# Optimization experiments

Measured on AMD Instinct MI355X. Metric: run time of the kernel, lower is better.

Reference implementation:

```python
import jax, jax.numpy as jnp
import numpy as np

LODS = [16, 32, 64, 128, 256]
SCENE_SCALE = 4.0
DESC = 4
N = 2_000_000
# 8 corner offsets of a voxel, bit-decoded: (x, y, z) in {0,1}^3
_CORNERS = jnp.asarray([[(i >> 2) & 1, (i >> 1) & 1, i & 1] for i in range(8)], dtype=jnp.int32)  # (8,3)


def setup_inputs() -> dict:
    key = jax.random.key(0)
    ks = jax.random.split(key, 2 + len(LODS))
    inp = {
        "pts": jax.random.normal(ks[0], (N, 3), dtype=jnp.float32),
        "d": jax.random.normal(ks[1], (N, 3), dtype=jnp.float32),
    }
    # codebook init mirrors torch: zeros + 0.01 * randn, shape (LOD^3, desc)
    for i, res in enumerate(LODS):
        inp[f"codebook_{i}"] = jax.random.normal(ks[2 + i], (res ** 3, DESC), dtype=jnp.float32) * 0.01
    return inp


def _trilerp(res, codebook, pts01):
    """NGLOD-style dense-grid trilinear interpolation.
    pts01: (N,3) in [0,1]; codebook: (res^3, DESC). Returns (N, DESC)."""
    pos = pts01 * (res - 1)                                   # (N,3) in [0, res-1]
    c0 = jnp.clip(jnp.floor(pos).astype(jnp.int32), 0, res - 2)
    frac = pos - c0.astype(pos.dtype)                         # (N,3) in [0,1]
    idx = c0[:, None, :] + _CORNERS[None, :, :]               # (N,8,3)
    flat = (idx[..., 0] * res + idx[..., 1]) * res + idx[..., 2]  # (N,8) row-major x*res^2+y*res+z
    # trilinear weights: prod over axes of (frac if corner bit set else 1-frac)
    w = jnp.prod(jnp.where(_CORNERS[None] == 1, frac[:, None, :], 1.0 - frac[:, None, :]), axis=-1)  # (N,8)
    return jnp.einsum('nkd,nk->nd', codebook[flat], w)        # gather + weighted sum


def reference(pts, d, codebook_0, codebook_1, codebook_2, codebook_3, codebook_4):
    cbs = (codebook_0, codebook_1, codebook_2, codebook_3, codebook_4)
    p = pts / SCENE_SCALE
    mask = jnp.all(jnp.abs(p) < 0.5, axis=-1)                 # inside unit cube
    p01 = jnp.clip(p + 0.5, 0.0, 1.0)                         # clamp keeps OOB points index-safe; masked out below
    feats = _trilerp(LODS[0], cbs[0], p01)
    for res, cb in zip(LODS[1:], cbs[1:]):
        feats = feats + _trilerp(res, cb, p01)                # sum features across LODs
    color = jnp.where(mask[:, None], feats[:, 0:3], 0.0)      # masked scatter into zero buffer
    log_sigma = jnp.where(mask, feats[:, 3], -100000.0)       # exp(-1e5) underflows to 0, as in torch
    return color, jnp.exp(log_sigma)[:, None]
```

## Files before the change

kernel.cpp:

```cpp
#include <hip/hip_runtime.h>
#include <math.h>

static constexpr float kSceneScale = 4.0f;
static constexpr int   kG     = 16;
static constexpr int   kNBins = kG * kG * kG + 1;
static constexpr int   kNB    = 256;
static constexpr int   kDirectThresh = 48;
static constexpr int   kS4    = 17;
static constexpr int   kChunk = 512;

__device__ __forceinline__ void fma4(float4& acc, float w, const float4& c) {
    acc.x = fmaf(w, c.x, acc.x);
    acc.y = fmaf(w, c.y, acc.y);
    acc.z = fmaf(w, c.z, acc.z);
    acc.w = fmaf(w, c.w, acc.w);
}

__device__ __forceinline__ unsigned bf16r(float f) {
    unsigned u = __float_as_uint(f);
    return (u + 0x7FFFu + ((u >> 16) & 1u)) >> 16;
}
__device__ __forceinline__ unsigned pk2(float lo, float hi) {
    return bf16r(lo) | (bf16r(hi) << 16);
}
__device__ __forceinline__ float4 bfdec(uint2 w) {
    float4 r;
    r.x = __uint_as_float(w.x << 16);
    r.y = __uint_as_float(w.x & 0xFFFF0000u);
    r.z = __uint_as_float(w.y << 16);
    r.w = __uint_as_float(w.y & 0xFFFF0000u);
    return r;
}

template <int RES>
__device__ __forceinline__ void trilerp_acc(const float4* __restrict__ cb,
                                            float x, float y, float z,
                                            float4& acc) {
    const float s = (float)(RES - 1);
    float fx = x * s, fy = y * s, fz = z * s;
    int x0 = min((int)fx, RES - 2);
    int y0 = min((int)fy, RES - 2);
    int z0 = min((int)fz, RES - 2);
    float tx = fx - (float)x0;
    float ty = fy - (float)y0;
    float tz = fz - (float)z0;
    int base = (x0 * RES + y0) * RES + z0;
    float4 c000 = cb[base];
    float4 c001 = cb[base + 1];
    float4 c010 = cb[base + RES];
    float4 c011 = cb[base + RES + 1];
    float4 c100 = cb[base + RES * RES];
    float4 c101 = cb[base + RES * RES + 1];
    float4 c110 = cb[base + RES * RES + RES];
    float4 c111 = cb[base + RES * RES + RES + 1];
    float wx0 = 1.0f - tx, wx1 = tx;
    float wy0 = 1.0f - ty, wy1 = ty;
    float wz0 = 1.0f - tz, wz1 = tz;
    fma4(acc, wx0 * wy0 * wz0, c000);
    fma4(acc, wx0 * wy0 * wz1, c001);
    fma4(acc, wx0 * wy1 * wz0, c010);
    fma4(acc, wx0 * wy1 * wz1, c011);
    fma4(acc, wx1 * wy0 * wz0, c100);
    fma4(acc, wx1 * wy0 * wz1, c101);
    fma4(acc, wx1 * wy1 * wz0, c110);
    fma4(acc, wx1 * wy1 * wz1, c111);
}

__device__ __forceinline__ void load_p01(const float* __restrict__ pts, int i,
                                         float& x, float& y, float& z, bool& inside) {
    float px = pts[3 * i + 0] * (1.0f / kSceneScale);
    float py = pts[3 * i + 1] * (1.0f / kSceneScale);
    float pz = pts[3 * i + 2] * (1.0f / kSceneScale);
    inside = (fabsf(px) < 0.5f) && (fabsf(py) < 0.5f) && (fabsf(pz) < 0.5f);
    x = fminf(fmaxf(px + 0.5f, 0.0f), 1.0f);
    y = fminf(fmaxf(py + 0.5f, 0.0f), 1.0f);
    z = fminf(fmaxf(pz + 0.5f, 0.0f), 1.0f);
}

__device__ __forceinline__ unsigned point_key(const float* __restrict__ pts, int i) {
    float x, y, z; bool inside;
    load_p01(pts, i, x, y, z, inside);
    if (!inside) return (unsigned)(kNBins - 1);
    int x0 = min((int)(x * 255.0f), 254) >> 4;
    int y0 = min((int)(y * 255.0f), 254) >> 4;
    int z0 = min((int)(z * 255.0f), 254) >> 4;
    return (unsigned)((x0 * kG + y0) * kG + z0);
}

__global__ __launch_bounds__(256) void keys_hist_kernel(
        const float* __restrict__ pts, unsigned* __restrict__ keys,
        unsigned* __restrict__ blockHist, int n, int chunk) {
    __shared__ unsigned hist[kNBins];
    int tid = threadIdx.x;
    for (int j = tid; j < kNBins; j += 256) hist[j] = 0;
    __syncthreads();
    int beg = blockIdx.x * chunk;
    int end = min(n, beg + chunk);
    for (int i = beg + tid; i < end; i += 256) {
        unsigned key = point_key(pts, i);
        keys[i] = key;
        atomicAdd(&hist[key], 1u);
    }
    __syncthreads();
    for (int j = tid; j < kNBins; j += 256) blockHist[(size_t)j * kNB + blockIdx.x] = hist[j];
}

__global__ __launch_bounds__(256) void scan_chunks_kernel(
        unsigned* __restrict__ data, unsigned* __restrict__ partials, int total) {
    __shared__ unsigned sums[256];
    int tid = threadIdx.x;
    int base = blockIdx.x * 1024 + tid * 4;
    uint4 v = make_uint4(0u, 0u, 0u, 0u);
    if (base + 3 < total) {
        v = *(const uint4*)(data + base);
    } else {
        unsigned* p = (unsigned*)&v;
        for (int k = 0; k < 4; ++k) if (base + k < total) p[k] = data[base + k];
    }
    unsigned s1 = v.x + v.y, s2 = s1 + v.z, s3 = s2 + v.w;
    sums[tid] = s3;
    __syncthreads();
    for (int off = 1; off < 256; off <<= 1) {
        unsigned t = (tid >= off) ? sums[tid - off] : 0u;
        __syncthreads();
        sums[tid] += t;
        __syncthreads();
    }
    unsigned excl = sums[tid] - s3;
    uint4 o;
    o.x = excl; o.y = excl + v.x; o.z = excl + s1; o.w = excl + s2;
    if (base + 3 < total) {
        *(uint4*)(data + base) = o;
    } else {
        unsigned* p = (unsigned*)&o;
        for (int k = 0; k < 4; ++k) if (base + k < total) data[base + k] = p[k];
    }
    if (tid == 255) partials[blockIdx.x] = sums[255];
}

__global__ __launch_bounds__(256) void scan_partials_kernel(unsigned* __restrict__ partials, int m) {
    __shared__ unsigned buf[256];
    __shared__ unsigned carry_s;
    int tid = threadIdx.x;
    if (tid == 0) carry_s = 0u;
    __syncthreads();
    for (int base = 0; base < m; base += 256) {
        unsigned v = (base + tid < m) ? partials[base + tid] : 0u;
        buf[tid] = v;
        __syncthreads();
        for (int off = 1; off < 256; off <<= 1) {
            unsigned t = (tid >= off) ? buf[tid - off] : 0u;
            __syncthreads();
            buf[tid] += t;
            __syncthreads();
        }
        unsigned incl = buf[tid];
        unsigned c = carry_s;
        if (base + tid < m) partials[base + tid] = c + incl - v;
        __syncthreads();
        if (tid == 255) carry_s = c + incl;
        __syncthreads();
    }
}

__global__ __launch_bounds__(256) void scan_add_kernel(
        unsigned* __restrict__ data, const unsigned* __restrict__ partials, int total) {
    int tid = threadIdx.x;
    int base = blockIdx.x * 1024 + tid * 4;
    unsigned p = partials[blockIdx.x];
    if (base + 3 < total) {
        uint4 v = *(const uint4*)(data + base);
        v.x += p; v.y += p; v.z += p; v.w += p;
        *(uint4*)(data + base) = v;
    } else {
        for (int k = 0; k < 4; ++k) if (base + k < total) data[base + k] += p;
    }
}

__global__ __launch_bounds__(256) void scatter_kernel(
        const float* __restrict__ pts,
        const unsigned* __restrict__ keys, const unsigned* __restrict__ blockHist,
        float4* __restrict__ spts, float* __restrict__ out, int n, int chunk) {
    __shared__ unsigned offs[kNBins];
    int tid = threadIdx.x;
    for (int j = tid; j < kNBins; j += 256) offs[j] = blockHist[(size_t)j * kNB + blockIdx.x];
    __syncthreads();
    int beg = blockIdx.x * chunk;
    int end = min(n, beg + chunk);
    for (int i = beg + tid; i < end; i += 256) {
        unsigned k = keys[i];
        float x, y, z; bool inside;
        load_p01(pts, i, x, y, z, inside);
        unsigned pos = atomicAdd(&offs[k], 1u);
        if (inside) {
            spts[pos] = make_float4(x, y, z, __uint_as_float((unsigned)i));
        } else {
            out[3 * i + 0] = 0.0f;
            out[3 * i + 1] = 0.0f;
            out[3 * i + 2] = 0.0f;
            out[(size_t)3 * n + i] = 0.0f;
        }
    }
}

__global__ __launch_bounds__(512) void build_work_kernel(
        const unsigned* __restrict__ blockHist,
        uint2* __restrict__ items, unsigned* __restrict__ numItems) {
    __shared__ unsigned counter;
    if (threadIdx.x == 0) counter = 0u;
    __syncthreads();
    for (int bin = threadIdx.x; bin < kG * kG * kG; bin += 512) {
        unsigned s = blockHist[(size_t)bin * kNB];
        unsigned e = blockHist[(size_t)(bin + 1) * kNB];
        unsigned cnt = e - s;
        if (cnt == 0u) continue;
        unsigned k = (cnt + kChunk - 1) / kChunk;
        unsigned base = atomicAdd(&counter, k);
        for (unsigned j = 0; j < k; ++j)
            items[base + j] = make_uint2((unsigned)bin, s + j * kChunk);
    }
    __syncthreads();
    if (threadIdx.x == 0) numItems[0] = counter;
}

__global__ __launch_bounds__(512, 8) void compute_tiled_kernel(
        const float4* __restrict__ spts,
        const unsigned* __restrict__ blockHist,
        const uint2* __restrict__ items,
        const unsigned* __restrict__ numItems,
        const float4* __restrict__ cb0,
        const float4* __restrict__ cb1,
        const float4* __restrict__ cb2,
        const float4* __restrict__ cb3,
        const float4* __restrict__ cb4,
        float* __restrict__ out,
        int n) {
    if (blockIdx.x >= numItems[0]) return;
    uint2 it = items[blockIdx.x];
    int bin = (int)it.x;
    unsigned start = it.y;
    unsigned binEnd = blockHist[(size_t)(bin + 1) * kNB];
    unsigned end = min(binEnd, start + (unsigned)kChunk);

    int tid = threadIdx.x;

    if ((int)(end - start) < kDirectThresh) {
        for (unsigned t = start + tid; t < end; t += 512) {
            float4 s = spts[t];
            int i = (int)__float_as_uint(s.w);
            float4 acc = make_float4(0.0f, 0.0f, 0.0f, 0.0f);
            trilerp_acc<16>(cb0, s.x, s.y, s.z, acc);
            trilerp_acc<32>(cb1, s.x, s.y, s.z, acc);
            trilerp_acc<64>(cb2, s.x, s.y, s.z, acc);
            trilerp_acc<128>(cb3, s.x, s.y, s.z, acc);
            trilerp_acc<256>(cb4, s.x, s.y, s.z, acc);
            out[3 * i + 0] = acc.x;
            out[3 * i + 1] = acc.y;
            out[3 * i + 2] = acc.z;
            out[(size_t)3 * n + i] = expf(acc.w);
        }
        return;
    }

    __shared__ uint2 s4[kS4 * kS4 * kS4];

    int bx = bin >> 8, by = (bin >> 4) & 15, bz = bin & 15;
    int ox = bx << 4, oy = by << 4, oz = bz << 4;

    for (int c = tid; c < kS4 * kS4 * kS4; c += 512) {
        int cz = c % kS4;
        int cy = (c / kS4) % kS4;
        int cx = c / (kS4 * kS4);
        int gx = min(ox + cx, 255);
        int gy = min(oy + cy, 255);
        int gz = min(oz + cz, 255);
        float4 v = cb4[((size_t)gx * 256 + gy) * 256 + gz];
        s4[c] = make_uint2(pk2(v.x, v.y), pk2(v.z, v.w));
    }
    __syncthreads();

    unsigned t = start + tid;
    if (t < end) {
        float4 s = spts[t];
        int i = (int)__float_as_uint(s.w);
        float4 acc = make_float4(0.0f, 0.0f, 0.0f, 0.0f);
        trilerp_acc<16>(cb0, s.x, s.y, s.z, acc);
        trilerp_acc<32>(cb1, s.x, s.y, s.z, acc);
        trilerp_acc<64>(cb2, s.x, s.y, s.z, acc);
        trilerp_acc<128>(cb3, s.x, s.y, s.z, acc);

        {
            float fx = s.x * 255.0f, fy = s.y * 255.0f, fz = s.z * 255.0f;
            int x0 = min((int)fx, 254);
            int y0 = min((int)fy, 254);
            int z0 = min((int)fz, 254);
            float tx = fx - (float)x0;
            float ty = fy - (float)y0;
            float tz = fz - (float)z0;
            int base = ((x0 - ox) * kS4 + (y0 - oy)) * kS4 + (z0 - oz);
            uint2 w000 = s4[base];
            uint2 w001 = s4[base + 1];
            uint2 w010 = s4[base + kS4];
            uint2 w011 = s4[base + kS4 + 1];
            uint2 w100 = s4[base + kS4 * kS4];
            uint2 w101 = s4[base + kS4 * kS4 + 1];
            uint2 w110 = s4[base + kS4 * kS4 + kS4];
            uint2 w111 = s4[base + kS4 * kS4 + kS4 + 1];
            float wx0 = 1.0f - tx, wx1 = tx;
            float wy0 = 1.0f - ty, wy1 = ty;
            float wz0 = 1.0f - tz, wz1 = tz;
            fma4(acc, wx0 * wy0 * wz0, bfdec(w000));
            fma4(acc, wx0 * wy0 * wz1, bfdec(w001));
            fma4(acc, wx0 * wy1 * wz0, bfdec(w010));
            fma4(acc, wx0 * wy1 * wz1, bfdec(w011));
            fma4(acc, wx1 * wy0 * wz0, bfdec(w100));
            fma4(acc, wx1 * wy0 * wz1, bfdec(w101));
            fma4(acc, wx1 * wy1 * wz0, bfdec(w110));
            fma4(acc, wx1 * wy1 * wz1, bfdec(w111));
        }

        out[3 * i + 0] = acc.x;
        out[3 * i + 1] = acc.y;
        out[3 * i + 2] = acc.z;
        out[(size_t)3 * n + i] = expf(acc.w);
    }
}

__global__ __launch_bounds__(256) void direct_kernel(
        const float* __restrict__ pts,
        const float4* __restrict__ cb0,
        const float4* __restrict__ cb1,
        const float4* __restrict__ cb2,
        const float4* __restrict__ cb3,
        const float4* __restrict__ cb4,
        float* __restrict__ out,
        int n) {
    int i = blockIdx.x * blockDim.x + threadIdx.x;
    if (i >= n) return;
    float x, y, z; bool inside;
    load_p01(pts, i, x, y, z, inside);
    float c0 = 0.0f, c1 = 0.0f, c2 = 0.0f, sg = 0.0f;
    if (inside) {
        float4 acc = make_float4(0.0f, 0.0f, 0.0f, 0.0f);
        trilerp_acc<16>(cb0, x, y, z, acc);
        trilerp_acc<32>(cb1, x, y, z, acc);
        trilerp_acc<64>(cb2, x, y, z, acc);
        trilerp_acc<128>(cb3, x, y, z, acc);
        trilerp_acc<256>(cb4, x, y, z, acc);
        c0 = acc.x; c1 = acc.y; c2 = acc.z; sg = expf(acc.w);
    }
    out[3 * i + 0] = c0;
    out[3 * i + 1] = c1;
    out[3 * i + 2] = c2;
    out[(size_t)3 * n + i] = sg;
}

extern "C" void kernel_launch(void* const* d_in, const int* in_sizes, int n_in,
                              void* d_out, int out_size, void* d_ws, size_t ws_size,
                              hipStream_t stream) {
    const float* pts = (const float*)d_in[0];
    const float4* cb0 = (const float4*)d_in[2];
    const float4* cb1 = (const float4*)d_in[3];
    const float4* cb2 = (const float4*)d_in[4];
    const float4* cb3 = (const float4*)d_in[5];
    const float4* cb4 = (const float4*)d_in[6];
    float* out = (float*)d_out;

    int n = in_sizes[0] / 3;

    const int histTotal = kNBins * kNB;
    const int nChunks   = (histTotal + 1023) / 1024;
    const int maxItems  = kG * kG * kG + (n + kChunk - 1) / kChunk;

    size_t off_keys  = 0;
    size_t off_spts  = (off_keys + (size_t)n * 4 + 15) & ~(size_t)15;
    size_t off_hist  = off_spts + (size_t)n * 16;
    size_t off_part  = off_hist + (size_t)histTotal * 4;
    size_t off_items = (off_part + (size_t)nChunks * 4 + 7) & ~(size_t)7;
    size_t off_nitem = off_items + (size_t)maxItems * 8;
    size_t need      = off_nitem + 4;

    dim3 block(256);
    int nwg = (n + 255) / 256;

    if (ws_size < need) {
        direct_kernel<<<dim3(nwg), block, 0, stream>>>(pts, cb0, cb1, cb2, cb3, cb4, out, n);
        return;
    }

    unsigned* keys      = (unsigned*)((char*)d_ws + off_keys);
    float4*   spts      = (float4*)((char*)d_ws + off_spts);
    unsigned* blockHist = (unsigned*)((char*)d_ws + off_hist);
    unsigned* partials  = (unsigned*)((char*)d_ws + off_part);
    uint2*    items     = (uint2*)((char*)d_ws + off_items);
    unsigned* numItems  = (unsigned*)((char*)d_ws + off_nitem);

    int chunk = (n + kNB - 1) / kNB;

    keys_hist_kernel<<<dim3(kNB), block, 0, stream>>>(pts, keys, blockHist, n, chunk);
    scan_chunks_kernel<<<dim3(nChunks), block, 0, stream>>>(blockHist, partials, histTotal);
    scan_partials_kernel<<<dim3(1), block, 0, stream>>>(partials, nChunks);
    scan_add_kernel<<<dim3(nChunks), block, 0, stream>>>(blockHist, partials, histTotal);
    scatter_kernel<<<dim3(kNB), block, 0, stream>>>(pts, keys, blockHist, spts, out, n, chunk);
    build_work_kernel<<<dim3(1), dim3(512), 0, stream>>>(blockHist, items, numItems);
    compute_tiled_kernel<<<dim3(maxItems), dim3(512), 0, stream>>>(
        spts, blockHist, items, numItems, cb0, cb1, cb2, cb3, cb4, out, n);
}
```

Baseline: 303.7 us.

## Stage all LOD codebook tiles in LDS and halve bin depth along z

The spatial bins are split twice as finely along z, with 8-voxel depth instead of 16. Each tiled block now stages bf16-packed codebook windows for all five LODs into shared memory, not only the finest one. The trilinear lookups for every level then read from LDS instead of issuing scattered global gathers for LODs 0-3. The trade-offs are twice as many histogram bins to scan, more staging work per block relative to its point count, and bf16 rounding on every level rather than just the finest.

```diff
diff --git a/kernel.cpp b/kernel.cpp
--- a/kernel.cpp
+++ b/kernel.cpp
@@ -2,11 +2,11 @@
 #include <math.h>
 
 static constexpr float kSceneScale = 4.0f;
-static constexpr int   kG     = 16;
-static constexpr int   kNBins = kG * kG * kG + 1;
+static constexpr int   kGX    = 16;
+static constexpr int   kGZ    = 32;
+static constexpr int   kNBins = kGX * kGX * kGZ + 1;
 static constexpr int   kNB    = 256;
 static constexpr int   kDirectThresh = 48;
-static constexpr int   kS4    = 17;
 static constexpr int   kChunk = 512;
 
 __device__ __forceinline__ void fma4(float4& acc, float w, const float4& c) {
@@ -83,8 +83,8 @@
     if (!inside) return (unsigned)(kNBins - 1);
     int x0 = min((int)(x * 255.0f), 254) >> 4;
     int y0 = min((int)(y * 255.0f), 254) >> 4;
-    int z0 = min((int)(z * 255.0f), 254) >> 4;
-    return (unsigned)((x0 * kG + y0) * kG + z0);
+    int z0 = min((int)(z * 255.0f), 254) >> 3;
+    return (unsigned)((x0 * kGX + y0) * kGZ + z0);
 }
 
 __global__ __launch_bounds__(256) void keys_hist_kernel(
@@ -209,7 +209,7 @@
     __shared__ unsigned counter;
     if (threadIdx.x == 0) counter = 0u;
     __syncthreads();
-    for (int bin = threadIdx.x; bin < kG * kG * kG; bin += 512) {
+    for (int bin = threadIdx.x; bin < kGX * kGX * kGZ; bin += 512) {
         unsigned s = blockHist[(size_t)bin * kNB];
         unsigned e = blockHist[(size_t)(bin + 1) * kNB];
         unsigned cnt = e - s;
@@ -222,6 +222,62 @@
     __syncthreads();
     if (threadIdx.x == 0) numItems[0] = counter;
 }
+
+template <int RES, int SX, int SZ>
+__device__ __forceinline__ void stage_lds(const float4* __restrict__ cb, uint2* sbuf,
+                                          int lox, int loy, int loz, int tid) {
+    constexpr int TOT = SX * SX * SZ;
+    for (int c = tid; c < TOT; c += 512) {
+        int cz = c % SZ;
+        int cy = (c / SZ) % SX;
+        int cx = c / (SZ * SX);
+        int gx = min(lox + cx, RES - 1);
+        int gy = min(loy + cy, RES - 1);
+        int gz = min(loz + cz, RES - 1);
+        float4 v = cb[((size_t)gx * RES + gy) * RES + gz];
+        sbuf[c] = make_uint2(pk2(v.x, v.y), pk2(v.z, v.w));
+    }
+}
+
+template <int RES, int SX, int SZ>
+__device__ __forceinline__ void lerp_lds(const uint2* sbuf,
+                                         int lox, int loy, int loz,
+                                         float x, float y, float z, float4& acc) {
+    const float s = (float)(RES - 1);
+    float fx = x * s, fy = y * s, fz = z * s;
+    int x0 = min((int)fx, RES - 2);
+    int y0 = min((int)fy, RES - 2);
+    int z0 = min((int)fz, RES - 2);
+    float tx = fx - (float)x0;
+    float ty = fy - (float)y0;
+    float tz = fz - (float)z0;
+    int base = ((x0 - lox) * SX + (y0 - loy)) * SZ + (z0 - loz);
+    uint2 w000 = sbuf[base];
+    uint2 w001 = sbuf[base + 1];
+    uint2 w010 = sbuf[base + SZ];
+    uint2 w011 = sbuf[base + SZ + 1];
+    uint2 w100 = sbuf[base + SZ * SX];
+    uint2 w101 = sbuf[base + SZ * SX + 1];
+    uint2 w110 = sbuf[base + SZ * SX + SZ];
+    uint2 w111 = sbuf[base + SZ * SX + SZ + 1];
+    float wx0 = 1.0f - tx, wx1 = tx;
+    float wy0 = 1.0f - ty, wy1 = ty;
+    float wz0 = 1.0f - tz, wz1 = tz;
+    fma4(acc, wx0 * wy0 * wz0, bfdec(w000));
+    fma4(acc, wx0 * wy0 * wz1, bfdec(w001));
+    fma4(acc, wx0 * wy1 * wz0, bfdec(w010));
+    fma4(acc, wx0 * wy1 * wz1, bfdec(w011));
+    fma4(acc, wx1 * wy0 * wz0, bfdec(w100));
+    fma4(acc, wx1 * wy0 * wz1, bfdec(w101));
+    fma4(acc, wx1 * wy1 * wz0, bfdec(w110));
+    fma4(acc, wx1 * wy1 * wz1, bfdec(w111));
+}
+
+static constexpr int kT4 = 17 * 17 * 9;
+static constexpr int kT3 = 10 * 10 * 6;
+static constexpr int kT2 = 6 * 6 * 4;
+static constexpr int kT1 = 4 * 4 * 3;
+static constexpr int kT0 = 3 * 3 * 3;
 
 __global__ __launch_bounds__(512, 8) void compute_tiled_kernel(
         const float4* __restrict__ spts,
@@ -262,21 +318,28 @@
         return;
     }
 
-    __shared__ uint2 s4[kS4 * kS4 * kS4];
-
-    int bx = bin >> 8, by = (bin >> 4) & 15, bz = bin & 15;
-    int ox = bx << 4, oy = by << 4, oz = bz << 4;
-
-    for (int c = tid; c < kS4 * kS4 * kS4; c += 512) {
-        int cz = c % kS4;
-        int cy = (c / kS4) % kS4;
-        int cx = c / (kS4 * kS4);
-        int gx = min(ox + cx, 255);
-        int gy = min(oy + cy, 255);
-        int gz = min(oz + cz, 255);
-        float4 v = cb4[((size_t)gx * 256 + gy) * 256 + gz];
-        s4[c] = make_uint2(pk2(v.x, v.y), pk2(v.z, v.w));
-    }
+    __shared__ uint2 s4[kT4];
+    __shared__ uint2 s3[kT3];
+    __shared__ uint2 s2[kT2];
+    __shared__ uint2 s1[kT1];
+    __shared__ uint2 s0[kT0];
+
+    int bz = bin % kGZ;
+    int by = (bin / kGZ) % kGX;
+    int bx = bin / (kGZ * kGX);
+    int ox4 = bx << 4, oy4 = by << 4, oz4 = bz << 3;
+
+    int lo4x = ox4,               lo4y = oy4,               lo4z = oz4;
+    int lo3x = (ox4 * 127) / 255, lo3y = (oy4 * 127) / 255, lo3z = (oz4 * 127) / 255;
+    int lo2x = (ox4 * 63) / 255,  lo2y = (oy4 * 63) / 255,  lo2z = (oz4 * 63) / 255;
+    int lo1x = (ox4 * 31) / 255,  lo1y = (oy4 * 31) / 255,  lo1z = (oz4 * 31) / 255;
+    int lo0x = (ox4 * 15) / 255,  lo0y = (oy4 * 15) / 255,  lo0z = (oz4 * 15) / 255;
+
+    stage_lds<256, 17, 9>(cb4, s4, lo4x, lo4y, lo4z, tid);
+    stage_lds<128, 10, 6>(cb3, s3, lo3x, lo3y, lo3z, tid);
+    stage_lds<64,  6,  4>(cb2, s2, lo2x, lo2y, lo2z, tid);
+    stage_lds<32,  4,  3>(cb1, s1, lo1x, lo1y, lo1z, tid);
+    stage_lds<16,  3,  3>(cb0, s0, lo0x, lo0y, lo0z, tid);
     __syncthreads();
 
     unsigned t = start + tid;
@@ -284,41 +347,11 @@
         float4 s = spts[t];
         int i = (int)__float_as_uint(s.w);
         float4 acc = make_float4(0.0f, 0.0f, 0.0f, 0.0f);
-        trilerp_acc<16>(cb0, s.x, s.y, s.z, acc);
-        trilerp_acc<32>(cb1, s.x, s.y, s.z, acc);
-        trilerp_acc<64>(cb2, s.x, s.y, s.z, acc);
-        trilerp_acc<128>(cb3, s.x, s.y, s.z, acc);
-
-        {
-            float fx = s.x * 255.0f, fy = s.y * 255.0f, fz = s.z * 255.0f;
-            int x0 = min((int)fx, 254);
-            int y0 = min((int)fy, 254);
-            int z0 = min((int)fz, 254);
-            float tx = fx - (float)x0;
-            float ty = fy - (float)y0;
-            float tz = fz - (float)z0;
-            int base = ((x0 - ox) * kS4 + (y0 - oy)) * kS4 + (z0 - oz);
-            uint2 w000 = s4[base];
-            uint2 w001 = s4[base + 1];
-            uint2 w010 = s4[base + kS4];
-            uint2 w011 = s4[base + kS4 + 1];
-            uint2 w100 = s4[base + kS4 * kS4];
-            uint2 w101 = s4[base + kS4 * kS4 + 1];
-            uint2 w110 = s4[base + kS4 * kS4 + kS4];
-            uint2 w111 = s4[base + kS4 * kS4 + kS4 + 1];
-            float wx0 = 1.0f - tx, wx1 = tx;
-            float wy0 = 1.0f - ty, wy1 = ty;
-            float wz0 = 1.0f - tz, wz1 = tz;
-            fma4(acc, wx0 * wy0 * wz0, bfdec(w000));
-            fma4(acc, wx0 * wy0 * wz1, bfdec(w001));
-            fma4(acc, wx0 * wy1 * wz0, bfdec(w010));
-            fma4(acc, wx0 * wy1 * wz1, bfdec(w011));
-            fma4(acc, wx1 * wy0 * wz0, bfdec(w100));
-            fma4(acc, wx1 * wy0 * wz1, bfdec(w101));
-            fma4(acc, wx1 * wy1 * wz0, bfdec(w110));
-            fma4(acc, wx1 * wy1 * wz1, bfdec(w111));
-        }
-
+        lerp_lds<16,  3,  3>(s0, lo0x, lo0y, lo0z, s.x, s.y, s.z, acc);
+        lerp_lds<32,  4,  3>(s1, lo1x, lo1y, lo1z, s.x, s.y, s.z, acc);
+        lerp_lds<64,  6,  4>(s2, lo2x, lo2y, lo2z, s.x, s.y, s.z, acc);
+        lerp_lds<128, 10, 6>(s3, lo3x, lo3y, lo3z, s.x, s.y, s.z, acc);
+        lerp_lds<256, 17, 9>(s4, lo4x, lo4y, lo4z, s.x, s.y, s.z, acc);
         out[3 * i + 0] = acc.x;
         out[3 * i + 1] = acc.y;
         out[3 * i + 2] = acc.z;
@@ -370,7 +403,7 @@
 
     const int histTotal = kNBins * kNB;
     const int nChunks   = (histTotal + 1023) / 1024;
-    const int maxItems  = kG * kG * kG + (n + kChunk - 1) / kChunk;
+    const int maxItems  = kGX * kGX * kGZ + (n + kChunk - 1) / kChunk;
 
     size_t off_keys  = 0;
     size_t off_spts  = (off_keys + (size_t)n * 4 + 15) & ~(size_t)15;
```

Measured after the change: 350.3 us. +15.3%, slower.
